# Kernel tuning notes

Measured on AMD Instinct MI355X. Metric: run time of the kernel, lower is better.

Reference implementation:

```python
import jax, jax.numpy as jnp
import numpy as np

B, EMBED, H, W = 2, 32, 96, 96
SQ = (4, 2); R = 2; EXP = 2
SCH = EMBED // SQ[0]            # 8  squeezed channel dim
SHSP = SCH * R * R              # 32 shuffled spatial dim
SSP = SHSP // SQ[1]             # 16 squeezed spatial dim (attention embed dim)
HEADS = SCH * EXP               # 16
EACH = SSP // SCH               # 2
IDX = np.array([i + j * SCH for i in range(SCH) for j in range(EACH)])
NIDX = np.array([i + j * EACH for i in range(EACH) for j in range(SCH)])


def conv(x, w, b, stride=1, pad=0, groups=1):
    y = jax.lax.conv_general_dilated(x, w, (stride, stride), [(pad, pad), (pad, pad)],
                                     feature_group_count=groups,
                                     dimension_numbers=('NCHW', 'OIHW', 'NCHW'))
    return y + b[None, :, None, None]


def ln_ch(x, w, b):
    # LayerNorm over channel dim (torch applies it on [B,HW,C])
    mu = x.mean(1, keepdims=True)
    var = ((x - mu) ** 2).mean(1, keepdims=True)
    return (x - mu) * jax.lax.rsqrt(var + 1e-5) * w[None, :, None, None] + b[None, :, None, None]


def l2n(x, axis):
    # F.normalize: divide by L2 norm clamped to eps
    return x / jnp.maximum(jnp.sqrt(jnp.sum(x * x, axis=axis, keepdims=True)), 1e-12)


def _qkv(x, wqkv, bqkv):
    Bb, C, Hh, Ww = x.shape
    qkv = conv(x, wqkv, bqkv, groups=C)                        # [B, C*EXP*3, H, W], per-channel 1x1
    qkv = qkv.reshape(Bb, C, EXP * 3, Hh, Ww).transpose(0, 2, 1, 3, 4)
    q, k, v = jnp.split(qkv, 3, axis=1)                        # each [B, EXP, C, H, W]
    hd = EXP * C // HEADS
    rs = lambda a: a.reshape(Bb, HEADS, hd, Hh * Ww)
    return rs(q), rs(k), rs(v)


def _fuse(o, wfus, bfus, Bb, C, Hh, Ww):
    o = o.reshape(Bb, EXP, C, Hh, Ww).transpose(0, 2, 1, 3, 4).reshape(Bb, C * EXP, Hh, Ww)
    return conv(o, wfus, bfus, groups=C)


def chan_attn(x, wqkv, bqkv, t, wfus, bfus):
    Bb, C, Hh, Ww = x.shape
    q, k, v = _qkv(x, wqkv, bqkv)
    q, k = l2n(q, -1), l2n(k, -1)
    a = jax.nn.softmax(jnp.einsum('bhdn,bhen->bhde', q, k) * t, axis=-1)   # [B,h,d,d]
    o = jnp.einsum('bhde,bhen->bhdn', a, v)
    return _fuse(o, wfus, bfus, Bb, C, Hh, Ww)


def spat_attn(x, wqkv, bqkv, t, wfus, bfus):
    Bb, C, Hh, Ww = x.shape
    q, k, v = _qkv(x, wqkv, bqkv)
    q, k = l2n(q, -2), l2n(k, -2)
    a = jax.nn.softmax(jnp.einsum('bhdn,bhdm->bhnm', q, k) * t, axis=-1)   # [B,h,HW,HW]
    o = jnp.einsum('bhnm,bhdm->bhdn', a, v)
    return _fuse(o, wfus, bfus, Bb, C, Hh, Ww)


def pixel_shuffle(x, r):
    Bb, C, Hh, Ww = x.shape
    x = x.reshape(Bb, C // (r * r), r, r, Hh, Ww).transpose(0, 1, 4, 2, 5, 3)
    return x.reshape(Bb, C // (r * r), Hh * r, Ww * r)


def _forward(x, ln1_w, ln1_b, cab_w1, cab_b1, cab_w2, cab_b2, cab_aw1, cab_ab1, cab_aw2, cab_ab2,
             sq1_w, sq1_b, sq2_w, sq2_b, ca_qkv_w, ca_qkv_b, ca_t, ca_fus_w, ca_fus_b,
             sa_qkv_w, sa_qkv_b, sa_t, sa_fus_w, sa_fus_b, un1_w, un1_b, un2_w, un2_b,
             ln2_w, ln2_b, da_w1, da_b1, da_dw_w, da_dw_b, da_pw, da_pb):
    Bb, C, Hh, Ww = x.shape
    xn = ln_ch(x, ln1_w, ln1_b)
    # ---- CAB branch (conv-GELU-conv + RCAN channel attention) ----
    c = jax.nn.gelu(conv(xn, cab_w1, cab_b1, pad=1), approximate=False)
    c = conv(c, cab_w2, cab_b2, pad=1)
    y = c.mean((2, 3), keepdims=True)
    y = jax.nn.relu(conv(y, cab_aw1, cab_ab1))
    y = jax.nn.sigmoid(conv(y, cab_aw2, cab_ab2))
    x_cab = c * y
    # ---- Condensed attention branch ----
    z = conv(xn, sq1_w, sq1_b)                                   # 1x1: C -> SCH
    z = conv(z, sq2_w, sq2_b, stride=R, groups=SCH)              # grouped RxR stride R: -> [B,SSP,H/R,W/R]
    z = z[:, IDX]
    z = chan_attn(z, ca_qkv_w, ca_qkv_b, ca_t, ca_fus_w, ca_fus_b)
    z = z[:, NIDX]
    z = spat_attn(z, sa_qkv_w, sa_qkv_b, sa_t, sa_fus_w, sa_fus_b)
    z = conv(z, un1_w, un1_b, groups=SCH)                        # SSP -> SHSP
    z = pixel_shuffle(z, R)                                      # -> [B,SCH,H,W]
    z = conv(z, un2_w, un2_b)                                    # SCH -> C
    x = x + z + x_cab
    # ---- Dual adaptive (gated depthwise-conv FFN) ----
    xn2 = ln_ch(x, ln2_w, ln2_b)
    d = conv(xn2, da_w1, da_b1)
    d = conv(d, da_dw_w, da_dw_b, pad=3, groups=C).reshape(Bb, C, 2, Hh, Ww)
    d = jax.nn.gelu(d[:, :, 0], approximate=False) * jax.nn.sigmoid(d[:, :, 1])
    d = conv(d, da_pw, da_pb)
    return x + d


def setup_inputs():
    key = jax.random.key(0)
    ks = iter(jax.random.split(key, 40))
    nrm = lambda s: jax.random.normal(next(ks), s, jnp.float32) * 0.05
    inp = {'x': jax.random.normal(next(ks), (B, EMBED, H, W), jnp.float32)}
    wshapes = {
        'cab_w1': (EMBED // 4, EMBED, 3, 3), 'cab_w2': (EMBED, EMBED // 4, 3, 3),
        'cab_aw1': (EMBED // 18, EMBED, 1, 1), 'cab_aw2': (EMBED, EMBED // 18, 1, 1),
        'sq1_w': (SCH, EMBED, 1, 1), 'sq2_w': (SSP, 1, R, R),
        'ca_qkv_w': (SSP * EXP * 3, 1, 1, 1), 'ca_fus_w': (SSP, EXP, 1, 1),
        'sa_qkv_w': (SSP * EXP * 3, 1, 1, 1), 'sa_fus_w': (SSP, EXP, 1, 1),
        'un1_w': (SHSP, SSP // SCH, 1, 1), 'un2_w': (EMBED, SCH, 1, 1),
        'da_w1': (EMBED, EMBED, 1, 1), 'da_dw_w': (2 * EMBED, 1, 7, 7), 'da_pw': (EMBED, EMBED, 1, 1),
    }
    bshapes = {'cab_b1': EMBED // 4, 'cab_b2': EMBED, 'cab_ab1': EMBED // 18, 'cab_ab2': EMBED,
               'sq1_b': SCH, 'sq2_b': SSP, 'ca_qkv_b': SSP * EXP * 3, 'ca_fus_b': SSP,
               'sa_qkv_b': SSP * EXP * 3, 'sa_fus_b': SSP, 'un1_b': SHSP, 'un2_b': EMBED,
               'da_b1': EMBED, 'da_dw_b': 2 * EMBED, 'da_pb': EMBED}
    for n, s in wshapes.items():
        inp[n] = nrm(s)
    for n, s in bshapes.items():
        inp[n] = nrm((s,))
    inp['ln1_w'] = jnp.ones((EMBED,), jnp.float32); inp['ln1_b'] = jnp.zeros((EMBED,), jnp.float32)
    inp['ln2_w'] = jnp.ones((EMBED,), jnp.float32); inp['ln2_b'] = jnp.zeros((EMBED,), jnp.float32)
    inp['ca_t'] = jnp.ones((1, HEADS, 1, 1), jnp.float32)
    inp['sa_t'] = jnp.ones((1, HEADS, 1, 1), jnp.float32)
    return inp


def reference(x, ln1_w, ln1_b, cab_w1, cab_b1, cab_w2, cab_b2, cab_aw1, cab_ab1, cab_aw2, cab_ab2,
              sq1_w, sq1_b, sq2_w, sq2_b, ca_qkv_w, ca_qkv_b, ca_t, ca_fus_w, ca_fus_b,
              sa_qkv_w, sa_qkv_b, sa_t, sa_fus_w, sa_fus_b, un1_w, un1_b, un2_w, un2_b,
              ln2_w, ln2_b, da_w1, da_b1, da_dw_w, da_dw_b, da_pw, da_pb):
    return _forward(x, ln1_w, ln1_b, cab_w1, cab_b1, cab_w2, cab_b2, cab_aw1, cab_ab1, cab_aw2, cab_ab2,
                    sq1_w, sq1_b, sq2_w, sq2_b, ca_qkv_w, ca_qkv_b, ca_t, ca_fus_w, ca_fus_b,
                    sa_qkv_w, sa_qkv_b, sa_t, sa_fus_w, sa_fus_b, un1_w, un1_b, un2_w, un2_b,
                    ln2_w, ln2_b, da_w1, da_b1, da_dw_w, da_dw_b, da_pw, da_pb)
```

## Files before the change

kernel.cpp:

```cpp
#include <hip/hip_runtime.h>
#include <cstdint>
#include <math.h>

#define NP 9216
#define NP2 2304
#define KH 12
#define NMOM 78

__device__ __forceinline__ float gelu_ex(float v){
  return 0.5f*v*(1.0f+erff(v*0.70710678118654752440f));
}
__device__ __forceinline__ float sigm(float v){
  return 1.0f/(1.0f+__expf(-v));
}

__global__ __launch_bounds__(256) void k_ln1(const float* __restrict__ x,
    const float* __restrict__ lw, const float* __restrict__ lb,
    const float* __restrict__ sw, const float* __restrict__ sb,
    float* __restrict__ xn, float* __restrict__ z1)
{
  __shared__ float sred[2][8][32];
  __shared__ float xnsh[32][33];
  int p = threadIdx.x & 31, sl = threadIdx.x >> 5;
  int pix = blockIdx.x*32 + p;
  int b = pix / NP, n = pix % NP;
  const float* xp = x + (size_t)b*32*NP + (size_t)(sl*4)*NP + n;
  float v[4]; float s=0.f, s2=0.f;
#pragma unroll
  for (int c=0;c<4;c++){ float t=xp[(size_t)c*NP]; v[c]=t; s+=t; s2+=t*t; }
  sred[0][sl][p]=s; sred[1][sl][p]=s2;
  __syncthreads();
  s=0.f; s2=0.f;
#pragma unroll
  for (int g=0;g<8;g++){ s += sred[0][g][p]; s2 += sred[1][g][p]; }
  float mu = s*(1.f/32.f);
  float var = s2*(1.f/32.f)-mu*mu;
  float rs = rsqrtf(var+1e-5f);
  float* xo = xn + (size_t)b*32*NP + (size_t)(sl*4)*NP + n;
#pragma unroll
  for (int c=0;c<4;c++){
    int cc = sl*4+c;
    float t = (v[c]-mu)*rs*lw[cc]+lb[cc];
    xo[(size_t)c*NP] = t;
    xnsh[p][cc] = t;
  }
  __syncthreads();
  float vv[32];
#pragma unroll
  for (int c=0;c<32;c++) vv[c]=xnsh[p][c];
  int g = sl;
  float a = sb[g];
#pragma unroll
  for (int c=0;c<32;c++) a += vv[c]*sw[g*32+c];
  z1[(size_t)b*8*NP + (size_t)g*NP + n] = a;
}

__global__ __launch_bounds__(256) void k_cab1(const float* __restrict__ xn,
    const float* __restrict__ w, const float* __restrict__ bias,
    float* __restrict__ c1)
{
  int og = blockIdx.x/72, pb = blockIdx.x%72;
  int idx = pb*256+threadIdx.x;
  int b = idx/NP, n = idx%NP, i = n/96, j = n%96;
  const float* xb = xn + (size_t)b*32*NP;
  const float* wb = w + og*288;
  int  o_[9]; float m_[9];
  int d=0;
#pragma unroll
  for (int di=0;di<3;di++){
    int ii=i+di-1; bool vi = (unsigned)ii<96u;
#pragma unroll
    for (int dj=0;dj<3;dj++){
      int jj=j+dj-1; bool v = vi && ((unsigned)jj<96u);
      o_[d] = v ? ii*96+jj : 0; m_[d] = v ? 1.f : 0.f; d++;
    }
  }
  float accd[9] = {0,0,0,0,0,0,0,0,0};
  for (int c=0;c<32;c++){
    const float* xp = xb + (size_t)c*NP;
    const float* wp = wb + c*9;
    float t[9];
#pragma unroll
    for (int d2=0;d2<9;d2++) t[d2] = xp[o_[d2]];
#pragma unroll
    for (int d2=0;d2<9;d2++) accd[d2] += t[d2]*wp[d2];
  }
  float acc = bias[og];
#pragma unroll
  for (int d2=0;d2<9;d2++) acc += accd[d2]*m_[d2];
  c1[(size_t)b*8*NP + (size_t)og*NP + n] = gelu_ex(acc);
}

__global__ __launch_bounds__(256) void k_cab2(const float* __restrict__ c1,
    const float* __restrict__ w, const float* __restrict__ bias,
    float* __restrict__ cbuf, float* __restrict__ ypart)
{
  int og = blockIdx.x/72, pb = blockIdx.x%72;
  int idx = pb*256+threadIdx.x;
  int b = idx/NP, n = idx%NP, i = n/96, j = n%96;
  const float* cb = c1 + (size_t)b*8*NP;
  int  o_[9]; float m_[9];
  int d=0;
#pragma unroll
  for (int di=0;di<3;di++){
    int ii=i+di-1; bool vi = (unsigned)ii<96u;
#pragma unroll
    for (int dj=0;dj<3;dj++){
      int jj=j+dj-1; bool v = vi && ((unsigned)jj<96u);
      o_[d] = v ? ii*96+jj : 0; m_[d] = v ? 1.f : 0.f; d++;
    }
  }
  float acc[4];
#pragma unroll
  for (int k=0;k<4;k++) acc[k]=bias[og*4+k];
  for (int c=0;c<8;c++){
    const float* xp = cb + (size_t)c*NP;
    float t[9];
#pragma unroll
    for (int d2=0;d2<9;d2++) t[d2] = xp[o_[d2]]*m_[d2];
#pragma unroll
    for (int k=0;k<4;k++){
      const float* wp = w + (og*4+k)*72 + c*9;
#pragma unroll
      for (int d2=0;d2<9;d2++) acc[k] += t[d2]*wp[d2];
    }
  }
  __shared__ float red[4][4];
  int wv = threadIdx.x>>6, ln = threadIdx.x&63;
#pragma unroll
  for (int k=0;k<4;k++){
    cbuf[(size_t)b*32*NP + (size_t)(og*4+k)*NP + n] = acc[k];
    float r = acc[k];
#pragma unroll
    for (int m=1;m<64;m<<=1) r += __shfl_xor(r, m, 64);
    if (ln==0) red[wv][k]=r;
  }
  __syncthreads();
  if (threadIdx.x<4){
    float r = red[0][threadIdx.x]+red[1][threadIdx.x]+red[2][threadIdx.x]+red[3][threadIdx.x];
    ypart[(og*72+pb)*4 + threadIdx.x] = r;
  }
}

__global__ __launch_bounds__(256) void k_sq2(const float* __restrict__ z1,
    const float* __restrict__ w, const float* __restrict__ bias,
    float* __restrict__ u, float* __restrict__ spart)
{
  int pr = blockIdx.x/18, pb = blockIdx.x%18;
  int idx = pb*256+threadIdx.x;
  int b = idx/NP2, n = idx%NP2, i = n/48, j = n%48;
  int ocA = pr, ocB = pr+8;
  int gA = ocA>>1, gB = ocB>>1;
  const float* zpA = z1 + ((size_t)b*8+gA)*NP + (size_t)(2*i)*96 + 2*j;
  const float* zpB = z1 + ((size_t)b*8+gB)*NP + (size_t)(2*i)*96 + 2*j;
  float vA = zpA[0]*w[ocA*4]+zpA[1]*w[ocA*4+1]+zpA[96]*w[ocA*4+2]+zpA[97]*w[ocA*4+3]+bias[ocA];
  float vB = zpB[0]*w[ocB*4]+zpB[1]*w[ocB*4+1]+zpB[96]*w[ocB*4+2]+zpB[97]*w[ocB*4+3]+bias[ocB];
  u[((size_t)b*16+2*pr)*NP2 + n]   = vA;
  u[((size_t)b*16+2*pr+1)*NP2 + n] = vB;
  __shared__ float red[4][5];
  int wv=threadIdx.x>>6, ln=threadIdx.x&63;
  float st[5]={vA,vB,vA*vA,vB*vB,vA*vB};
#pragma unroll
  for (int k=0;k<5;k++){
    float r=st[k];
#pragma unroll
    for (int m=1;m<64;m<<=1) r+=__shfl_xor(r,m,64);
    if (ln==0) red[wv][k]=r;
  }
  __syncthreads();
  if (threadIdx.x<5){
    float r = red[0][threadIdx.x]+red[1][threadIdx.x]+red[2][threadIdx.x]+red[3][threadIdx.x];
    spart[(b*9 + (pb%9))*40 + pr*5 + threadIdx.x] = r;
  }
}

__global__ __launch_bounds__(256) void k_qkmom(const float* __restrict__ u,
    const float* __restrict__ spart,
    const float* __restrict__ cqw, const float* __restrict__ cqb,
    const float* __restrict__ cat, const float* __restrict__ cfw,
    const float* __restrict__ cfb,
    const float* __restrict__ qw, const float* __restrict__ qb,
    float2* __restrict__ qarr, float* __restrict__ mompart)
{
  int bh = blockIdx.x/9, ch = blockIdx.x%9;
  int n = ch*256 + threadIdx.x;
  int b = bh>>4, h = bh&15;
  int p = h&7, s = h>>3;
  int cc0=2*p, cc1=2*p+1;
  int oc0 = 2*(cc0&7)+(cc0>>3);
  int oc1 = 2*(cc1&7)+(cc1>>3);
  float AA[2], BB[2], CCc[2];
#pragma unroll
  for (int t2=0;t2<2;t2++){
    int oc = t2? oc1:oc0;
    int p2 = oc>>1, dd = oc&1;
    float st[5]={0,0,0,0,0};
    for (int ib=0; ib<9; ib++){
#pragma unroll
      for (int k=0;k<5;k++) st[k] += spart[(b*9+ib)*40 + p2*5 + k];
    }
    float S0=st[0],S1=st[1],Q00=st[2],Q11=st[3],Q01=st[4];
    float Sd = dd? S1:S0;
    float Qdd = dd? Q11:Q00;
    float cu0[2],cu1[2],ccst[2];
#pragma unroll
    for (int hh=0;hh<2;hh++){
      int h2=p2+8*hh;
      float th2=cat[h2];
      float aq=cqw[(2*p2+dd)*6+hh], bq=cqb[(2*p2+dd)*6+hh];
      float nq=fmaxf(sqrtf(fmaxf(aq*aq*Qdd+2.f*aq*bq*Sd+2304.f*bq*bq,0.f)),1e-12f);
      float m2[2],av[2],bv[2];
#pragma unroll
      for (int e=0;e<2;e++){
        float Se_=e?S1:S0, Qee=e?Q11:Q00, Qde=(dd==e)?Qdd:Q01;
        float ak=cqw[(2*p2+e)*6+2+hh], bk=cqb[(2*p2+e)*6+2+hh];
        float nk=fmaxf(sqrtf(fmaxf(ak*ak*Qee+2.f*ak*bk*Se_+2304.f*bk*bk,0.f)),1e-12f);
        float D=aq*ak*Qde + aq*bk*Sd + bq*ak*Se_ + 2304.f*bq*bk;
        m2[e]=th2*D/(nq*nk);
        av[e]=cqw[(2*p2+e)*6+4+hh]; bv[e]=cqb[(2*p2+e)*6+4+hh];
      }
      float mx=fmaxf(m2[0],m2[1]);
      float e0=__expf(m2[0]-mx), e1=__expf(m2[1]-mx);
      float inv=1.f/(e0+e1);
      cu0[hh]=e0*inv*av[0]; cu1[hh]=e1*inv*av[1]; ccst[hh]=e0*inv*bv[0]+e1*inv*bv[1];
    }
    float f0=cfw[oc*2], f1=cfw[oc*2+1];
    AA[t2]=f0*cu0[0]+f1*cu0[1];
    BB[t2]=f0*cu1[0]+f1*cu1[1];
    CCc[t2]=f0*ccst[0]+f1*ccst[1]+cfb[oc];
  }
  const float* u00 = u + ((size_t)b*16 + (oc0>>1)*2)*NP2;
  const float* u01 = u00 + NP2;
  const float* u10 = u + ((size_t)b*16 + (oc1>>1)*2)*NP2;
  const float* u11 = u10 + NP2;
  float w0 = AA[0]*u00[n]+BB[0]*u01[n]+CCc[0];
  float w1 = AA[1]*u10[n]+BB[1]*u11[n]+CCc[1];
  float k0 = qw[cc0*6+2+s]*w0+qb[cc0*6+2+s];
  float k1 = qw[cc1*6+2+s]*w1+qb[cc1*6+2+s];
  float rnk = 1.f/fmaxf(sqrtf(k0*k0+k1*k1),1e-12f);
  float kc = k0*rnk, ks = k1*rnk;
  float q0 = qw[cc0*6+s]*w0+qb[cc0*6+s];
  float q1 = qw[cc1*6+s]*w1+qb[cc1*6+s];
  float rnq = 1.f/fmaxf(sqrtf(q0*q0+q1*q1),1e-12f);
  qarr[bh*NP2+n] = make_float2(q0*rnq, q1*rnq);

  __shared__ float red[16][80];
  int grp = threadIdx.x>>4, gl = threadIdx.x&15;
  float c = 1.f, sn = 0.f;
#pragma unroll
  for (int k=0;k<=KH;k++){
    float vals[6] = {c, sn, c*w0, sn*w0, c*w1, sn*w1};
#pragma unroll
    for (int j=0;j<6;j++){
      float r = vals[j];
      r += __shfl_xor(r, 1, 64);
      r += __shfl_xor(r, 2, 64);
      r += __shfl_xor(r, 4, 64);
      r += __shfl_xor(r, 8, 64);
      if (gl==0) red[grp][k*6+j] = r;
    }
    float cn = c*kc - sn*ks;
    sn = sn*kc + c*ks;
    c = cn;
  }
  __syncthreads();
  if (threadIdx.x < NMOM){
    float r = 0.f;
#pragma unroll
    for (int g=0;g<16;g++) r += red[g][threadIdx.x];
    mompart[(bh*9+ch)*NMOM + threadIdx.x] = r;
  }
}

__global__ __launch_bounds__(256) void k_rows(const float2* __restrict__ qarr,
    const float* __restrict__ mompart, const float* __restrict__ sat,
    const float* __restrict__ qw, const float* __restrict__ qb,
    const float* __restrict__ fw, const float* __restrict__ fb,
    const float* __restrict__ u1w, const float* __restrict__ u1b,
    float* __restrict__ ps)
{
  int bp = blockIdx.x/9, ch = blockIdx.x%9;
  int b = bp>>3, p = bp&7;
  int n = ch*256 + (int)threadIdx.x;
  __shared__ float msh[2][80];
  __shared__ float fsh[2][13];
  int tid = threadIdx.x;
  if (tid < 26){
    int hh = tid/13, k = tid%13;
    double t = (double)sat[p+8*hh];
    double fac;
    if (fabs(t) < 1e-3){
      double xh = 0.5*t;
      double pk = 1.0;
      for (int q=1;q<=k;q++) pk *= xh/(double)q;
      double Ik = pk*(1.0 + xh*xh/(double)(k+1));
      fac = (k? 2.0:1.0)*Ik;
    } else {
      const int KS = 36;
      double ip1 = 0.0, ik = 1e-280, sum2 = 0.0;
      double vk = 0.0, v0 = 0.0;
      for (int q=KS; q>=1; --q){
        if (q == k) vk = ik;
        sum2 += ik;
        double im1 = ip1 + (2.0*(double)q/t)*ik;
        ip1 = ik; ik = im1;
      }
      v0 = ik;
      if (k == 0) vk = v0;
      double total = v0 + 2.0*sum2;
      double scale = exp(t)/total;
      fac = (k? 2.0:1.0)*vk*scale;
    }
    fsh[hh][k] = (float)fac;
  }
  if (tid < 2*NMOM){
    int hh = tid/NMOM, jj = tid%NMOM;
    float ssum = 0.f;
    for (int ib=0; ib<9; ib++)
      ssum += mompart[((size_t)(b*16+p+8*hh)*9+ib)*NMOM + jj];
    msh[hh][jj] = ssum;
  }
  __syncthreads();
  if (tid < 2*NMOM){
    int hh = tid/NMOM, jj = tid%NMOM;
    msh[hh][jj] *= fsh[hh][jj/6];
  }
  __syncthreads();
  float o[2][2];
#pragma unroll
  for (int hh=0;hh<2;hh++){
    float2 q = qarr[(size_t)(b*16+p+8*hh)*NP2 + n];
    float c = 1.f, sn = 0.f;
    float Se=0.f, S0=0.f, S1=0.f;
#pragma unroll
    for (int k=0;k<=KH;k++){
      const float* mk = &msh[hh][k*6];
      Se += c*mk[0] + sn*mk[1];
      S0 += c*mk[2] + sn*mk[3];
      S1 += c*mk[4] + sn*mk[5];
      float cn = c*q.x - sn*q.y;
      sn = sn*q.x + c*q.y;
      c = cn;
    }
    float rSe = 1.f/Se;
    float av0=qw[(2*p)*6+4+hh],  bv0=qb[(2*p)*6+4+hh];
    float av1=qw[(2*p+1)*6+4+hh],bv1=qb[(2*p+1)*6+4+hh];
    o[hh][0]=av0*S0*rSe+bv0;
    o[hh][1]=av1*S1*rSe+bv1;
  }
  float zz0 = o[0][0]*fw[(2*p)*2]   + o[1][0]*fw[(2*p)*2+1]   + fb[2*p];
  float zz1 = o[0][1]*fw[(2*p+1)*2] + o[1][1]*fw[(2*p+1)*2+1] + fb[2*p+1];
  int i=n/48, j=n%48;
  float* pb = ps + ((size_t)b*8+p)*NP;
#pragma unroll
  for (int k=0;k<4;k++){
    int od = 4*p+k;
    float v = zz0*u1w[od*2] + zz1*u1w[od*2+1] + u1b[od];
    pb[(size_t)(2*i+(k>>1))*96 + 2*j + (k&1)] = v;
  }
}

__global__ __launch_bounds__(256) void k_un2(const float* __restrict__ ps,
    const float* __restrict__ ypart,
    const float* __restrict__ aw1, const float* __restrict__ ab1,
    const float* __restrict__ aw2, const float* __restrict__ ab2,
    const float* __restrict__ u2w, const float* __restrict__ u2b,
    const float* __restrict__ x, const float* __restrict__ cbuf,
    const float* __restrict__ lw, const float* __restrict__ lb,
    const float* __restrict__ dw1, const float* __restrict__ db1,
    float* __restrict__ xsum, float* __restrict__ d1)
{
  __shared__ float sred[2][8][32];
  __shared__ float xsh[32][33];
  __shared__ float y2sh[32];
  int p = threadIdx.x & 31, sl = threadIdx.x >> 5;
  int pix = blockIdx.x*32 + p;
  int b = pix/NP, n = pix%NP;
  if (threadIdx.x < 32){
    int c = threadIdx.x;
    float ssum = 0.f;
    for (int ib=0; ib<36; ib++)
      ssum += ypart[((c>>2)*72 + b*36 + ib)*4 + (c&3)];
    float pr = ssum*(1.f/9216.f)*aw1[c];
#pragma unroll
    for (int m=1;m<32;m<<=1) pr += __shfl_xor(pr, m, 64);
    float y1 = fmaxf(pr+ab1[0], 0.f);
    y2sh[c] = sigm(aw2[c]*y1+ab2[c]);
  }
  float pg[8];
#pragma unroll
  for (int g=0;g<8;g++) pg[g]=ps[((size_t)b*8+g)*NP+n];
  __syncthreads();
  float xv[4]; float s=0.f,s2=0.f;
#pragma unroll
  for (int c=0;c<4;c++){
    int cc = sl*4+c;
    float a=u2b[cc];
#pragma unroll
    for (int g=0;g<8;g++) a+=pg[g]*u2w[cc*8+g];
    size_t off=((size_t)b*32+cc)*NP+n;
    float t = x[off]+a+cbuf[off]*y2sh[cc];
    xv[c]=t; xsum[off]=t; s+=t; s2+=t*t;
  }
  sred[0][sl][p]=s; sred[1][sl][p]=s2;
  __syncthreads();
  s=0.f; s2=0.f;
#pragma unroll
  for (int g=0;g<8;g++){ s += sred[0][g][p]; s2 += sred[1][g][p]; }
  float mu=s*(1.f/32.f), var=s2*(1.f/32.f)-mu*mu, rs=rsqrtf(var+1e-5f);
#pragma unroll
  for (int c=0;c<4;c++){
    int cc = sl*4+c;
    xsh[p][cc] = (xv[c]-mu)*rs*lw[cc]+lb[cc];
  }
  __syncthreads();
  float vv[32];
#pragma unroll
  for (int c=0;c<32;c++) vv[c]=xsh[p][c];
#pragma unroll
  for (int k=0;k<4;k++){
    int o = sl*4+k;
    float a=db1[o];
#pragma unroll
    for (int cc=0;cc<32;cc++) a+=vv[cc]*dw1[o*32+cc];
    d1[((size_t)b*32+o)*NP+n]=a;
  }
}

__global__ __launch_bounds__(256) void k_dw(const float* __restrict__ d1,
    const float* __restrict__ w, const float* __restrict__ bias,
    float* __restrict__ dg)
{
  int idx = blockIdx.x*256+threadIdx.x;
  int pl = idx/4608, n2 = idx%4608;
  int i2 = n2/96, j = n2%96;
  int c = pl&31;
  const float* dp = d1 + (size_t)pl*NP;
  const float* w0p = w + (2*c)*49;
  const float* w1p = w + (2*c+1)*49;
  float a0=bias[2*c], a1=bias[2*c+1];
  float c0=bias[2*c], c1=bias[2*c+1];
#pragma unroll
  for (int di=0;di<8;di++){
    int ii=2*i2-3+di; if ((unsigned)ii>=96u) continue;
    const float* rowp = dp + ii*96;
    float t[7];
#pragma unroll
    for (int dj=0;dj<7;dj++){
      int jj=j+dj-3;
      t[dj] = ((unsigned)jj<96u) ? rowp[jj] : 0.f;
    }
    if (di<7){
#pragma unroll
      for (int dj=0;dj<7;dj++){ a0 += t[dj]*w0p[di*7+dj]; a1 += t[dj]*w1p[di*7+dj]; }
    }
    if (di>0){
#pragma unroll
      for (int dj=0;dj<7;dj++){ c0 += t[dj]*w0p[(di-1)*7+dj]; c1 += t[dj]*w1p[(di-1)*7+dj]; }
    }
  }
  dg[(size_t)pl*NP + (size_t)(2*i2)*96 + j]   = gelu_ex(a0)*sigm(a1);
  dg[(size_t)pl*NP + (size_t)(2*i2+1)*96 + j] = gelu_ex(c0)*sigm(c1);
}

__global__ __launch_bounds__(256) void k_fin(const float* __restrict__ dg,
    const float* __restrict__ pw, const float* __restrict__ pb,
    const float* __restrict__ xsum, float* __restrict__ out)
{
  __shared__ float xsh[32][33];
  int p = threadIdx.x & 31, sl = threadIdx.x >> 5;
  int pix = blockIdx.x*32 + p;
  int b = pix/NP, n = pix%NP;
  const float* dp = dg + ((size_t)b*32 + sl*4)*NP + n;
#pragma unroll
  for (int c=0;c<4;c++) xsh[p][sl*4+c]=dp[(size_t)c*NP];
  __syncthreads();
  float vv[32];
#pragma unroll
  for (int c=0;c<32;c++) vv[c]=xsh[p][c];
#pragma unroll
  for (int k=0;k<4;k++){
    int o = sl*4+k;
    float a=pb[o];
#pragma unroll
    for (int cc=0;cc<32;cc++) a+=vv[cc]*pw[o*32+cc];
    size_t off=((size_t)b*32+o)*NP+n;
    out[off]=xsum[off]+a;
  }
}

extern "C" void kernel_launch(void* const* d_in, const int* in_sizes, int n_in,
                              void* d_out, int out_size, void* d_ws, size_t ws_size,
                              hipStream_t stream) {
  (void)in_sizes; (void)n_in; (void)out_size; (void)ws_size;
  const float* x       =(const float*)d_in[0];
  const float* cab_w1  =(const float*)d_in[1];
  const float* cab_w2  =(const float*)d_in[2];
  const float* cab_aw1 =(const float*)d_in[3];
  const float* cab_aw2 =(const float*)d_in[4];
  const float* sq1_w   =(const float*)d_in[5];
  const float* sq2_w   =(const float*)d_in[6];
  const float* ca_qkv_w=(const float*)d_in[7];
  const float* ca_fus_w=(const float*)d_in[8];
  const float* sa_qkv_w=(const float*)d_in[9];
  const float* sa_fus_w=(const float*)d_in[10];
  const float* un1_w   =(const float*)d_in[11];
  const float* un2_w   =(const float*)d_in[12];
  const float* da_w1   =(const float*)d_in[13];
  const float* da_dw_w =(const float*)d_in[14];
  const float* da_pw   =(const float*)d_in[15];
  const float* cab_b1  =(const float*)d_in[16];
  const float* cab_b2  =(const float*)d_in[17];
  const float* cab_ab1 =(const float*)d_in[18];
  const float* cab_ab2 =(const float*)d_in[19];
  const float* sq1_b   =(const float*)d_in[20];
  const float* sq2_b   =(const float*)d_in[21];
  const float* ca_qkv_b=(const float*)d_in[22];
  const float* ca_fus_b=(const float*)d_in[23];
  const float* sa_qkv_b=(const float*)d_in[24];
  const float* sa_fus_b=(const float*)d_in[25];
  const float* un1_b   =(const float*)d_in[26];
  const float* un2_b   =(const float*)d_in[27];
  const float* da_b1   =(const float*)d_in[28];
  const float* da_dw_b =(const float*)d_in[29];
  const float* da_pb   =(const float*)d_in[30];
  const float* ln1_w   =(const float*)d_in[31];
  const float* ln1_b   =(const float*)d_in[32];
  const float* ln2_w   =(const float*)d_in[33];
  const float* ln2_b   =(const float*)d_in[34];
  const float* ca_t    =(const float*)d_in[35];
  const float* sa_t    =(const float*)d_in[36];

  float* ws=(float*)d_ws;
  float* xn    = ws;
  float* z1    = ws + 589824;
  float* c1b   = ws + 737280;
  float* cb    = ws + 884736;
  float* u     = ws + 1474560;
  float* psb   = ws + 1548288;
  float* xsm   = ws + 1695744;
  float* ypart = ws + 2285568;
  float* spart = ws + 2287872;
  float2* qarr = (float2*)(ws + 2288640);
  float* mompart = ws + 2436096;
  float* d1    = xn;
  float* dg    = cb;

  k_ln1  <<<576, 256,0,stream>>>(x, ln1_w, ln1_b, sq1_w, sq1_b, xn, z1);
  k_cab1 <<<576, 256,0,stream>>>(xn, cab_w1, cab_b1, c1b);
  k_cab2 <<<576, 256,0,stream>>>(c1b, cab_w2, cab_b2, cb, ypart);
  k_sq2  <<<144, 256,0,stream>>>(z1, sq2_w, sq2_b, u, spart);
  k_qkmom<<<288, 256,0,stream>>>(u, spart, ca_qkv_w, ca_qkv_b, ca_t, ca_fus_w, ca_fus_b,
                                 sa_qkv_w, sa_qkv_b, qarr, mompart);
  k_rows <<<144, 256,0,stream>>>(qarr, mompart, sa_t, sa_qkv_w, sa_qkv_b,
                                 sa_fus_w, sa_fus_b, un1_w, un1_b, psb);
  k_un2  <<<576, 256,0,stream>>>(psb, ypart, cab_aw1, cab_ab1, cab_aw2, cab_ab2,
                                 un2_w, un2_b, x, cb, ln2_w, ln2_b, da_w1, da_b1, xsm, d1);
  k_dw   <<<1152,256,0,stream>>>(d1, da_dw_w, da_dw_b, dg);
  k_fin  <<<576, 256,0,stream>>>(dg, da_pw, da_pb, xsm, (float*)d_out);
}
```

Baseline: 86.11 us.

## Merge independent conv and squeeze stages into shared launches, restructure conv loops

Merges k_cab1 with k_sq2 into one launch (k_phB) and k_cab2 with k_qkmom into another (k_phC), dispatching on block index, because these branches do not depend on each other. This removes two kernel launches and the gaps between them, and lets the small attention kernels run alongside the conv blocks. The 3x3 conv loops are also reordered to iterate over taps first and skip out-of-bounds taps with branches, replacing the masked loads and multiplies. Risks: warp divergence at image borders, and shared-memory and register usage in each merged kernel being the maximum of its two branches, which can lower occupancy.

```diff
diff --git a/kernel.cpp b/kernel.cpp
--- a/kernel.cpp
+++ b/kernel.cpp
@@ -55,220 +55,202 @@
   z1[(size_t)b*8*NP + (size_t)g*NP + n] = a;
 }
 
-__global__ __launch_bounds__(256) void k_cab1(const float* __restrict__ xn,
-    const float* __restrict__ w, const float* __restrict__ bias,
-    float* __restrict__ c1)
-{
-  int og = blockIdx.x/72, pb = blockIdx.x%72;
-  int idx = pb*256+threadIdx.x;
-  int b = idx/NP, n = idx%NP, i = n/96, j = n%96;
-  const float* xb = xn + (size_t)b*32*NP;
-  const float* wb = w + og*288;
-  int  o_[9]; float m_[9];
-  int d=0;
-#pragma unroll
-  for (int di=0;di<3;di++){
-    int ii=i+di-1; bool vi = (unsigned)ii<96u;
-#pragma unroll
-    for (int dj=0;dj<3;dj++){
-      int jj=j+dj-1; bool v = vi && ((unsigned)jj<96u);
-      o_[d] = v ? ii*96+jj : 0; m_[d] = v ? 1.f : 0.f; d++;
-    }
-  }
-  float accd[9] = {0,0,0,0,0,0,0,0,0};
-  for (int c=0;c<32;c++){
-    const float* xp = xb + (size_t)c*NP;
-    const float* wp = wb + c*9;
-    float t[9];
-#pragma unroll
-    for (int d2=0;d2<9;d2++) t[d2] = xp[o_[d2]];
-#pragma unroll
-    for (int d2=0;d2<9;d2++) accd[d2] += t[d2]*wp[d2];
-  }
-  float acc = bias[og];
-#pragma unroll
-  for (int d2=0;d2<9;d2++) acc += accd[d2]*m_[d2];
-  c1[(size_t)b*8*NP + (size_t)og*NP + n] = gelu_ex(acc);
-}
-
-__global__ __launch_bounds__(256) void k_cab2(const float* __restrict__ c1,
-    const float* __restrict__ w, const float* __restrict__ bias,
-    float* __restrict__ cbuf, float* __restrict__ ypart)
-{
-  int og = blockIdx.x/72, pb = blockIdx.x%72;
-  int idx = pb*256+threadIdx.x;
-  int b = idx/NP, n = idx%NP, i = n/96, j = n%96;
-  const float* cb = c1 + (size_t)b*8*NP;
-  int  o_[9]; float m_[9];
-  int d=0;
-#pragma unroll
-  for (int di=0;di<3;di++){
-    int ii=i+di-1; bool vi = (unsigned)ii<96u;
-#pragma unroll
-    for (int dj=0;dj<3;dj++){
-      int jj=j+dj-1; bool v = vi && ((unsigned)jj<96u);
-      o_[d] = v ? ii*96+jj : 0; m_[d] = v ? 1.f : 0.f; d++;
-    }
-  }
-  float acc[4];
-#pragma unroll
-  for (int k=0;k<4;k++) acc[k]=bias[og*4+k];
-  for (int c=0;c<8;c++){
-    const float* xp = cb + (size_t)c*NP;
-    float t[9];
-#pragma unroll
-    for (int d2=0;d2<9;d2++) t[d2] = xp[o_[d2]]*m_[d2];
-#pragma unroll
-    for (int k=0;k<4;k++){
-      const float* wp = w + (og*4+k)*72 + c*9;
-#pragma unroll
-      for (int d2=0;d2<9;d2++) acc[k] += t[d2]*wp[d2];
-    }
-  }
-  __shared__ float red[4][4];
-  int wv = threadIdx.x>>6, ln = threadIdx.x&63;
-#pragma unroll
-  for (int k=0;k<4;k++){
-    cbuf[(size_t)b*32*NP + (size_t)(og*4+k)*NP + n] = acc[k];
-    float r = acc[k];
-#pragma unroll
-    for (int m=1;m<64;m<<=1) r += __shfl_xor(r, m, 64);
-    if (ln==0) red[wv][k]=r;
-  }
-  __syncthreads();
-  if (threadIdx.x<4){
-    float r = red[0][threadIdx.x]+red[1][threadIdx.x]+red[2][threadIdx.x]+red[3][threadIdx.x];
-    ypart[(og*72+pb)*4 + threadIdx.x] = r;
-  }
-}
-
-__global__ __launch_bounds__(256) void k_sq2(const float* __restrict__ z1,
-    const float* __restrict__ w, const float* __restrict__ bias,
-    float* __restrict__ u, float* __restrict__ spart)
-{
-  int pr = blockIdx.x/18, pb = blockIdx.x%18;
-  int idx = pb*256+threadIdx.x;
-  int b = idx/NP2, n = idx%NP2, i = n/48, j = n%48;
-  int ocA = pr, ocB = pr+8;
-  int gA = ocA>>1, gB = ocB>>1;
-  const float* zpA = z1 + ((size_t)b*8+gA)*NP + (size_t)(2*i)*96 + 2*j;
-  const float* zpB = z1 + ((size_t)b*8+gB)*NP + (size_t)(2*i)*96 + 2*j;
-  float vA = zpA[0]*w[ocA*4]+zpA[1]*w[ocA*4+1]+zpA[96]*w[ocA*4+2]+zpA[97]*w[ocA*4+3]+bias[ocA];
-  float vB = zpB[0]*w[ocB*4]+zpB[1]*w[ocB*4+1]+zpB[96]*w[ocB*4+2]+zpB[97]*w[ocB*4+3]+bias[ocB];
-  u[((size_t)b*16+2*pr)*NP2 + n]   = vA;
-  u[((size_t)b*16+2*pr+1)*NP2 + n] = vB;
-  __shared__ float red[4][5];
-  int wv=threadIdx.x>>6, ln=threadIdx.x&63;
-  float st[5]={vA,vB,vA*vA,vB*vB,vA*vB};
-#pragma unroll
-  for (int k=0;k<5;k++){
-    float r=st[k];
-#pragma unroll
-    for (int m=1;m<64;m<<=1) r+=__shfl_xor(r,m,64);
-    if (ln==0) red[wv][k]=r;
-  }
-  __syncthreads();
-  if (threadIdx.x<5){
-    float r = red[0][threadIdx.x]+red[1][threadIdx.x]+red[2][threadIdx.x]+red[3][threadIdx.x];
-    spart[(b*9 + (pb%9))*40 + pr*5 + threadIdx.x] = r;
-  }
-}
-
-__global__ __launch_bounds__(256) void k_qkmom(const float* __restrict__ u,
-    const float* __restrict__ spart,
+__global__ __launch_bounds__(256) void k_phB(const float* __restrict__ xn,
+    const float* __restrict__ w1, const float* __restrict__ b1,
+    const float* __restrict__ z1, const float* __restrict__ w2,
+    const float* __restrict__ b2,
+    float* __restrict__ c1, float* __restrict__ u, float* __restrict__ spart)
+{
+  if (blockIdx.x < 576){
+    int og = blockIdx.x/72, pb = blockIdx.x%72;
+    int idx = pb*256+threadIdx.x;
+    int b = idx/NP, n = idx%NP, i = n/96, j = n%96;
+    float acc = b1[og];
+    const float* xb = xn + (size_t)b*32*NP;
+    const float* wb = w1 + og*288;
+#pragma unroll
+    for (int di=0;di<3;di++){
+      int ii=i+di-1; if ((unsigned)ii>=96u) continue;
+#pragma unroll
+      for (int dj=0;dj<3;dj++){
+        int jj=j+dj-1; if ((unsigned)jj>=96u) continue;
+        const float* xp = xb + ii*96+jj;
+        const float* wp = wb + di*3+dj;
+#pragma unroll
+        for (int c=0;c<32;c++) acc += xp[(size_t)c*NP]*wp[c*9];
+      }
+    }
+    c1[(size_t)b*8*NP + (size_t)og*NP + n] = gelu_ex(acc);
+  } else {
+    __shared__ float red[4][5];
+    int u2 = blockIdx.x-576;
+    int pr = u2/18, pb = u2%18;
+    int idx = pb*256+threadIdx.x;
+    int b = idx/NP2, n = idx%NP2, i = n/48, j = n%48;
+    int ocA = pr, ocB = pr+8;
+    int gA = ocA>>1, gB = ocB>>1;
+    const float* zpA = z1 + ((size_t)b*8+gA)*NP + (size_t)(2*i)*96 + 2*j;
+    const float* zpB = z1 + ((size_t)b*8+gB)*NP + (size_t)(2*i)*96 + 2*j;
+    float vA = zpA[0]*w2[ocA*4]+zpA[1]*w2[ocA*4+1]+zpA[96]*w2[ocA*4+2]+zpA[97]*w2[ocA*4+3]+b2[ocA];
+    float vB = zpB[0]*w2[ocB*4]+zpB[1]*w2[ocB*4+1]+zpB[96]*w2[ocB*4+2]+zpB[97]*w2[ocB*4+3]+b2[ocB];
+    u[((size_t)b*16+2*pr)*NP2 + n]   = vA;
+    u[((size_t)b*16+2*pr+1)*NP2 + n] = vB;
+    int wv=threadIdx.x>>6, ln=threadIdx.x&63;
+    float st[5]={vA,vB,vA*vA,vB*vB,vA*vB};
+#pragma unroll
+    for (int k=0;k<5;k++){
+      float r=st[k];
+#pragma unroll
+      for (int m=1;m<64;m<<=1) r+=__shfl_xor(r,m,64);
+      if (ln==0) red[wv][k]=r;
+    }
+    __syncthreads();
+    if (threadIdx.x<5){
+      float r = red[0][threadIdx.x]+red[1][threadIdx.x]+red[2][threadIdx.x]+red[3][threadIdx.x];
+      spart[(b*9 + (pb%9))*40 + pr*5 + threadIdx.x] = r;
+    }
+  }
+}
+
+__global__ __launch_bounds__(256) void k_phC(const float* __restrict__ c1,
+    const float* __restrict__ w2, const float* __restrict__ b2,
+    float* __restrict__ cbuf, float* __restrict__ ypart,
+    const float* __restrict__ u, const float* __restrict__ spart,
     const float* __restrict__ cqw, const float* __restrict__ cqb,
     const float* __restrict__ cat, const float* __restrict__ cfw,
     const float* __restrict__ cfb,
     const float* __restrict__ qw, const float* __restrict__ qb,
     float2* __restrict__ qarr, float* __restrict__ mompart)
 {
-  int bh = blockIdx.x/9, ch = blockIdx.x%9;
-  int n = ch*256 + threadIdx.x;
-  int b = bh>>4, h = bh&15;
-  int p = h&7, s = h>>3;
-  int cc0=2*p, cc1=2*p+1;
-  int oc0 = 2*(cc0&7)+(cc0>>3);
-  int oc1 = 2*(cc1&7)+(cc1>>3);
-  float AA[2], BB[2], CCc[2];
-#pragma unroll
-  for (int t2=0;t2<2;t2++){
-    int oc = t2? oc1:oc0;
-    int p2 = oc>>1, dd = oc&1;
-    float st[5]={0,0,0,0,0};
-    for (int ib=0; ib<9; ib++){
-#pragma unroll
-      for (int k=0;k<5;k++) st[k] += spart[(b*9+ib)*40 + p2*5 + k];
-    }
-    float S0=st[0],S1=st[1],Q00=st[2],Q11=st[3],Q01=st[4];
-    float Sd = dd? S1:S0;
-    float Qdd = dd? Q11:Q00;
-    float cu0[2],cu1[2],ccst[2];
-#pragma unroll
-    for (int hh=0;hh<2;hh++){
-      int h2=p2+8*hh;
-      float th2=cat[h2];
-      float aq=cqw[(2*p2+dd)*6+hh], bq=cqb[(2*p2+dd)*6+hh];
-      float nq=fmaxf(sqrtf(fmaxf(aq*aq*Qdd+2.f*aq*bq*Sd+2304.f*bq*bq,0.f)),1e-12f);
-      float m2[2],av[2],bv[2];
-#pragma unroll
-      for (int e=0;e<2;e++){
-        float Se_=e?S1:S0, Qee=e?Q11:Q00, Qde=(dd==e)?Qdd:Q01;
-        float ak=cqw[(2*p2+e)*6+2+hh], bk=cqb[(2*p2+e)*6+2+hh];
-        float nk=fmaxf(sqrtf(fmaxf(ak*ak*Qee+2.f*ak*bk*Se_+2304.f*bk*bk,0.f)),1e-12f);
-        float D=aq*ak*Qde + aq*bk*Sd + bq*ak*Se_ + 2304.f*bq*bk;
-        m2[e]=th2*D/(nq*nk);
-        av[e]=cqw[(2*p2+e)*6+4+hh]; bv[e]=cqb[(2*p2+e)*6+4+hh];
+  if (blockIdx.x < 576){
+    __shared__ float red[4][4];
+    int og = blockIdx.x/72, pb = blockIdx.x%72;
+    int idx = pb*256+threadIdx.x;
+    int b = idx/NP, n = idx%NP, i = n/96, j = n%96;
+    float acc[4];
+#pragma unroll
+    for (int k=0;k<4;k++) acc[k]=b2[og*4+k];
+    const float* cb = c1 + (size_t)b*8*NP;
+#pragma unroll
+    for (int di=0;di<3;di++){
+      int ii=i+di-1; if ((unsigned)ii>=96u) continue;
+#pragma unroll
+      for (int dj=0;dj<3;dj++){
+        int jj=j+dj-1; if ((unsigned)jj>=96u) continue;
+        const float* xp = cb + ii*96+jj;
+#pragma unroll
+        for (int c=0;c<8;c++){
+          float val = xp[(size_t)c*NP];
+          const float* wp = w2 + (og*4)*72 + c*9+di*3+dj;
+#pragma unroll
+          for (int k=0;k<4;k++) acc[k] += val*wp[k*72];
+        }
       }
-      float mx=fmaxf(m2[0],m2[1]);
-      float e0=__expf(m2[0]-mx), e1=__expf(m2[1]-mx);
-      float inv=1.f/(e0+e1);
-      cu0[hh]=e0*inv*av[0]; cu1[hh]=e1*inv*av[1]; ccst[hh]=e0*inv*bv[0]+e1*inv*bv[1];
-    }
-    float f0=cfw[oc*2], f1=cfw[oc*2+1];
-    AA[t2]=f0*cu0[0]+f1*cu0[1];
-    BB[t2]=f0*cu1[0]+f1*cu1[1];
-    CCc[t2]=f0*ccst[0]+f1*ccst[1]+cfb[oc];
-  }
-  const float* u00 = u + ((size_t)b*16 + (oc0>>1)*2)*NP2;
-  const float* u01 = u00 + NP2;
-  const float* u10 = u + ((size_t)b*16 + (oc1>>1)*2)*NP2;
-  const float* u11 = u10 + NP2;
-  float w0 = AA[0]*u00[n]+BB[0]*u01[n]+CCc[0];
-  float w1 = AA[1]*u10[n]+BB[1]*u11[n]+CCc[1];
-  float k0 = qw[cc0*6+2+s]*w0+qb[cc0*6+2+s];
-  float k1 = qw[cc1*6+2+s]*w1+qb[cc1*6+2+s];
-  float rnk = 1.f/fmaxf(sqrtf(k0*k0+k1*k1),1e-12f);
-  float kc = k0*rnk, ks = k1*rnk;
-  float q0 = qw[cc0*6+s]*w0+qb[cc0*6+s];
-  float q1 = qw[cc1*6+s]*w1+qb[cc1*6+s];
-  float rnq = 1.f/fmaxf(sqrtf(q0*q0+q1*q1),1e-12f);
-  qarr[bh*NP2+n] = make_float2(q0*rnq, q1*rnq);
-
-  __shared__ float red[16][80];
-  int grp = threadIdx.x>>4, gl = threadIdx.x&15;
-  float c = 1.f, sn = 0.f;
-#pragma unroll
-  for (int k=0;k<=KH;k++){
-    float vals[6] = {c, sn, c*w0, sn*w0, c*w1, sn*w1};
-#pragma unroll
-    for (int j=0;j<6;j++){
-      float r = vals[j];
-      r += __shfl_xor(r, 1, 64);
-      r += __shfl_xor(r, 2, 64);
-      r += __shfl_xor(r, 4, 64);
-      r += __shfl_xor(r, 8, 64);
-      if (gl==0) red[grp][k*6+j] = r;
-    }
-    float cn = c*kc - sn*ks;
-    sn = sn*kc + c*ks;
-    c = cn;
-  }
-  __syncthreads();
-  if (threadIdx.x < NMOM){
-    float r = 0.f;
-#pragma unroll
-    for (int g=0;g<16;g++) r += red[g][threadIdx.x];
-    mompart[(bh*9+ch)*NMOM + threadIdx.x] = r;
+    }
+    int wv = threadIdx.x>>6, ln = threadIdx.x&63;
+#pragma unroll
+    for (int k=0;k<4;k++){
+      cbuf[(size_t)b*32*NP + (size_t)(og*4+k)*NP + n] = acc[k];
+      float r = acc[k];
+#pragma unroll
+      for (int m=1;m<64;m<<=1) r += __shfl_xor(r, m, 64);
+      if (ln==0) red[wv][k]=r;
+    }
+    __syncthreads();
+    if (threadIdx.x<4){
+      float r = red[0][threadIdx.x]+red[1][threadIdx.x]+red[2][threadIdx.x]+red[3][threadIdx.x];
+      ypart[(og*72+pb)*4 + threadIdx.x] = r;
+    }
+  } else {
+    __shared__ float red16[16][80];
+    int u2 = blockIdx.x-576;
+    int bh = u2/9, ch = u2%9;
+    int n = ch*256 + threadIdx.x;
+    int b = bh>>4, h = bh&15;
+    int p = h&7, s = h>>3;
+    int cc0=2*p, cc1=2*p+1;
+    int oc0 = 2*(cc0&7)+(cc0>>3);
+    int oc1 = 2*(cc1&7)+(cc1>>3);
+    float AA[2], BB[2], CCc[2];
+#pragma unroll
+    for (int t2=0;t2<2;t2++){
+      int oc = t2? oc1:oc0;
+      int p2 = oc>>1, dd = oc&1;
+      float st[5]={0,0,0,0,0};
+      for (int ib=0; ib<9; ib++){
+#pragma unroll
+        for (int k=0;k<5;k++) st[k] += spart[(b*9+ib)*40 + p2*5 + k];
+      }
+      float S0=st[0],S1=st[1],Q00=st[2],Q11=st[3],Q01=st[4];
+      float Sd = dd? S1:S0;
+      float Qdd = dd? Q11:Q00;
+      float cu0[2],cu1[2],ccst[2];
+#pragma unroll
+      for (int hh=0;hh<2;hh++){
+        int h2=p2+8*hh;
+        float th2=cat[h2];
+        float aq=cqw[(2*p2+dd)*6+hh], bq=cqb[(2*p2+dd)*6+hh];
+        float nq=fmaxf(sqrtf(fmaxf(aq*aq*Qdd+2.f*aq*bq*Sd+2304.f*bq*bq,0.f)),1e-12f);
+        float m2[2],av[2],bv[2];
+#pragma unroll
+        for (int e=0;e<2;e++){
+          float Se_=e?S1:S0, Qee=e?Q11:Q00, Qde=(dd==e)?Qdd:Q01;
+          float ak=cqw[(2*p2+e)*6+2+hh], bk=cqb[(2*p2+e)*6+2+hh];
+          float nk=fmaxf(sqrtf(fmaxf(ak*ak*Qee+2.f*ak*bk*Se_+2304.f*bk*bk,0.f)),1e-12f);
+          float D=aq*ak*Qde + aq*bk*Sd + bq*ak*Se_ + 2304.f*bq*bk;
+          m2[e]=th2*D/(nq*nk);
+          av[e]=cqw[(2*p2+e)*6+4+hh]; bv[e]=cqb[(2*p2+e)*6+4+hh];
+        }
+        float mx=fmaxf(m2[0],m2[1]);
+        float e0=__expf(m2[0]-mx), e1=__expf(m2[1]-mx);
+        float inv=1.f/(e0+e1);
+        cu0[hh]=e0*inv*av[0]; cu1[hh]=e1*inv*av[1]; ccst[hh]=e0*inv*bv[0]+e1*inv*bv[1];
+      }
+      float f0=cfw[oc*2], f1=cfw[oc*2+1];
+      AA[t2]=f0*cu0[0]+f1*cu0[1];
+      BB[t2]=f0*cu1[0]+f1*cu1[1];
+      CCc[t2]=f0*ccst[0]+f1*ccst[1]+cfb[oc];
+    }
+    const float* u00 = u + ((size_t)b*16 + (oc0>>1)*2)*NP2;
+    const float* u01 = u00 + NP2;
+    const float* u10 = u + ((size_t)b*16 + (oc1>>1)*2)*NP2;
+    const float* u11 = u10 + NP2;
+    float w0 = AA[0]*u00[n]+BB[0]*u01[n]+CCc[0];
+    float w1 = AA[1]*u10[n]+BB[1]*u11[n]+CCc[1];
+    float k0 = qw[cc0*6+2+s]*w0+qb[cc0*6+2+s];
+    float k1 = qw[cc1*6+2+s]*w1+qb[cc1*6+2+s];
+    float rnk = 1.f/fmaxf(sqrtf(k0*k0+k1*k1),1e-12f);
+    float kc = k0*rnk, ks = k1*rnk;
+    float q0 = qw[cc0*6+s]*w0+qb[cc0*6+s];
+    float q1 = qw[cc1*6+s]*w1+qb[cc1*6+s];
+    float rnq = 1.f/fmaxf(sqrtf(q0*q0+q1*q1),1e-12f);
+    qarr[bh*NP2+n] = make_float2(q0*rnq, q1*rnq);
+
+    int grp = threadIdx.x>>4, gl = threadIdx.x&15;
+    float c = 1.f, sn = 0.f;
+#pragma unroll
+    for (int k=0;k<=KH;k++){
+      float vals[6] = {c, sn, c*w0, sn*w0, c*w1, sn*w1};
+#pragma unroll
+      for (int jv=0;jv<6;jv++){
+        float r = vals[jv];
+        r += __shfl_xor(r, 1, 64);
+        r += __shfl_xor(r, 2, 64);
+        r += __shfl_xor(r, 4, 64);
+        r += __shfl_xor(r, 8, 64);
+        if (gl==0) red16[grp][k*6+jv] = r;
+      }
+      float cn = c*kc - sn*ks;
+      sn = sn*kc + c*ks;
+      c = cn;
+    }
+    __syncthreads();
+    if (threadIdx.x < NMOM){
+      float r = 0.f;
+#pragma unroll
+      for (int g=0;g<16;g++) r += red16[g][threadIdx.x];
+      mompart[(bh*9+ch)*NMOM + threadIdx.x] = r;
+    }
   }
 }
 
@@ -351,12 +333,12 @@
   float zz0 = o[0][0]*fw[(2*p)*2]   + o[1][0]*fw[(2*p)*2+1]   + fb[2*p];
   float zz1 = o[0][1]*fw[(2*p+1)*2] + o[1][1]*fw[(2*p+1)*2+1] + fb[2*p+1];
   int i=n/48, j=n%48;
-  float* pb = ps + ((size_t)b*8+p)*NP;
+  float* pb2 = ps + ((size_t)b*8+p)*NP;
 #pragma unroll
   for (int k=0;k<4;k++){
     int od = 4*p+k;
     float v = zz0*u1w[od*2] + zz1*u1w[od*2+1] + u1b[od];
-    pb[(size_t)(2*i+(k>>1))*96 + 2*j + (k&1)] = v;
+    pb2[(size_t)(2*i+(k>>1))*96 + 2*j + (k&1)] = v;
   }
 }
 
@@ -546,16 +528,15 @@
   float* d1    = xn;
   float* dg    = cb;
 
-  k_ln1  <<<576, 256,0,stream>>>(x, ln1_w, ln1_b, sq1_w, sq1_b, xn, z1);
-  k_cab1 <<<576, 256,0,stream>>>(xn, cab_w1, cab_b1, c1b);
-  k_cab2 <<<576, 256,0,stream>>>(c1b, cab_w2, cab_b2, cb, ypart);
-  k_sq2  <<<144, 256,0,stream>>>(z1, sq2_w, sq2_b, u, spart);
-  k_qkmom<<<288, 256,0,stream>>>(u, spart, ca_qkv_w, ca_qkv_b, ca_t, ca_fus_w, ca_fus_b,
-                                 sa_qkv_w, sa_qkv_b, qarr, mompart);
-  k_rows <<<144, 256,0,stream>>>(qarr, mompart, sa_t, sa_qkv_w, sa_qkv_b,
-                                 sa_fus_w, sa_fus_b, un1_w, un1_b, psb);
-  k_un2  <<<576, 256,0,stream>>>(psb, ypart, cab_aw1, cab_ab1, cab_aw2, cab_ab2,
-                                 un2_w, un2_b, x, cb, ln2_w, ln2_b, da_w1, da_b1, xsm, d1);
-  k_dw   <<<1152,256,0,stream>>>(d1, da_dw_w, da_dw_b, dg);
-  k_fin  <<<576, 256,0,stream>>>(dg, da_pw, da_pb, xsm, (float*)d_out);
-}
+  k_ln1 <<<576, 256,0,stream>>>(x, ln1_w, ln1_b, sq1_w, sq1_b, xn, z1);
+  k_phB <<<720, 256,0,stream>>>(xn, cab_w1, cab_b1, z1, sq2_w, sq2_b, c1b, u, spart);
+  k_phC <<<864, 256,0,stream>>>(c1b, cab_w2, cab_b2, cb, ypart,
+                                u, spart, ca_qkv_w, ca_qkv_b, ca_t, ca_fus_w, ca_fus_b,
+                                sa_qkv_w, sa_qkv_b, qarr, mompart);
+  k_rows<<<144, 256,0,stream>>>(qarr, mompart, sa_t, sa_qkv_w, sa_qkv_b,
+                                sa_fus_w, sa_fus_b, un1_w, un1_b, psb);
+  k_un2 <<<576, 256,0,stream>>>(psb, ypart, cab_aw1, cab_ab1, cab_aw2, cab_ab2,
+                                un2_w, un2_b, x, cb, ln2_w, ln2_b, da_w1, da_b1, xsm, d1);
+  k_dw  <<<1152,256,0,stream>>>(d1, da_dw_w, da_dw_b, dg);
+  k_fin <<<576, 256,0,stream>>>(dg, da_pw, da_pb, xsm, (float*)d_out);
+}
```

After: 71.43 us, median of 5. 1.21x faster.
